# Performance work log

Hardware: AMD Instinct MI355X
Metric: run time of the kernel (lower is better)

Reference implementation:

```python
import jax, jax.numpy as jnp
import numpy as np

L = 262144      # number of points
C = 256         # in_channels
NH = 8          # num_heads
G = 64          # group_size
FF = 2048       # torch TransformerEncoderLayer default dim_feedforward
LPAD = 262144   # padded length, divisible by G; LPAD//G divisible by batch_size
BS = 4


def setup_inputs() -> dict:
    key = jax.random.key(0)
    ks = jax.random.split(key, 12)
    def w(k, shape, scale=0.02):
        return jax.random.normal(k, shape, jnp.float32) * scale
    return {
        "feats_flat": jax.random.normal(ks[0], (L, C), jnp.float32),
        "x_idx": jax.random.randint(ks[1], (L,), 0, L),
        "flat2win": jax.random.randint(ks[2], (LPAD,), 0, L),
        "win2flat": jax.random.randint(ks[3], (L,), 0, LPAD),
        "in_proj_w": w(ks[4], (3 * C, C)),
        "in_proj_b": jnp.zeros((3 * C,), jnp.float32),
        "out_proj_w": w(ks[5], (C, C)),
        "out_proj_b": jnp.zeros((C,), jnp.float32),
        "lin1_w": w(ks[6], (FF, C)),
        "lin1_b": jnp.zeros((FF,), jnp.float32),
        "lin2_w": w(ks[7], (C, FF)),
        "lin2_b": jnp.zeros((C,), jnp.float32),
        "ln1_g": jnp.ones((C,), jnp.float32),
        "ln1_b": jnp.zeros((C,), jnp.float32),
        "ln2_g": jnp.ones((C,), jnp.float32),
        "ln2_b": jnp.zeros((C,), jnp.float32),
        "proj_w": w(ks[8], (C, 2 * C)),
        "proj_b": jnp.zeros((C,), jnp.float32),
        "batch_size": BS,
    }


def _layer_norm(x, g, b, eps=1e-5):
    mu = jnp.mean(x, axis=-1, keepdims=True)
    var = jnp.var(x, axis=-1, keepdims=True)
    return (x - mu) * jax.lax.rsqrt(var + eps) * g + b


def _mha(x, in_proj_w, in_proj_b, out_proj_w, out_proj_b):
    B, S, Cm = x.shape
    hd = Cm // NH
    qkv = x @ in_proj_w.T + in_proj_b                      # [B,S,3C]
    q, k, v = jnp.split(qkv, 3, axis=-1)
    q = q.reshape(B, S, NH, hd)
    k = k.reshape(B, S, NH, hd)
    v = v.reshape(B, S, NH, hd)
    scores = jnp.einsum("bqhd,bkhd->bhqk", q, k) / jnp.sqrt(jnp.float32(hd))
    attn = jax.nn.softmax(scores, axis=-1)
    out = jnp.einsum("bhqk,bkhd->bqhd", attn, v).reshape(B, S, Cm)
    return out @ out_proj_w.T + out_proj_b


def reference(feats_flat, x_idx, flat2win, win2flat,
              in_proj_w, in_proj_b, out_proj_w, out_proj_b,
              lin1_w, lin1_b, lin2_w, lin2_b,
              ln1_g, ln1_b, ln2_g, ln2_b,
              proj_w, proj_b, batch_size):
    Cc = feats_flat.shape[1]
    # gather: feats_flat[indices][flat2win] -> [NW, G, C]
    feats_win = feats_flat[x_idx][flat2win].reshape(-1, G, Cc)
    # adaptive max pool over the group axis -> [NW, C]
    feats_pool = jnp.max(feats_win, axis=1)
    # torch TransformerEncoderLayer (post-norm, relu, eval/no-dropout)
    x = feats_pool.reshape(batch_size, -1, Cc)             # [B, S, C]
    x = _layer_norm(x + _mha(x, in_proj_w, in_proj_b, out_proj_w, out_proj_b), ln1_g, ln1_b)
    ff = jax.nn.relu(x @ lin1_w.T + lin1_b) @ lin2_w.T + lin2_b
    x = _layer_norm(x + ff, ln2_g, ln2_b)
    feats_global = x.reshape(-1, Cc)                       # [NW, C]
    # broadcast global feature to every group element, concat (global first)
    fuse_in = jnp.concatenate(
        [jnp.broadcast_to(feats_global[:, None, :], feats_win.shape), feats_win],
        axis=-1)                                           # [NW, G, 2C]
    feats_fuse = (fuse_in @ proj_w.T + proj_b).reshape(-1, Cc)  # [LPAD, C]
    # scatter back: feats_flat[indices] = feats_fuse[win2flat]
    return feats_flat.at[x_idx].set(feats_fuse[win2flat])
```

## Files before the change

kernel.cpp:

```cpp
#include <hip/hip_runtime.h>
#include <math.h>

namespace {
constexpr int kL    = 262144;
constexpr int kC    = 256;
constexpr int kNH   = 8;
constexpr int kG    = 64;
constexpr int kFF   = 2048;
constexpr int kLPAD = 262144;
constexpr int kBS   = 4;
constexpr int kNW   = kLPAD / kG;
constexpr int kS    = kNW / kBS;
constexpr int kHD   = kC / kNH;

constexpr size_t MB        = 1024 * 1024;
constexpr size_t OFF_GIDX   = 0;
constexpr size_t OFF_WINNER = 1 * MB;
constexpr size_t OFF_WLIST  = 2 * MB;
constexpr size_t OFF_CNT    = 3 * MB;
constexpr size_t OFF_X0     = 4 * MB;
constexpr size_t OFF_BASE   = 8 * MB;
constexpr size_t OFF_QKV    = 8 * MB;
constexpr size_t OFF_ATTN   = 20 * MB;
constexpr size_t OFF_X2     = 20 * MB;
constexpr size_t OFF_Y      = 24 * MB;
constexpr size_t OFF_X1     = 28 * MB;
constexpr size_t OFF_FF1    = 32 * MB;
constexpr size_t OFF_WINB   = 64 * MB;
constexpr size_t OFF_WOUTB  = OFF_WINB  + 512 * 1024;
constexpr size_t OFF_W1B    = OFF_WOUTB + 256 * 1024;
constexpr size_t OFF_W2B    = OFF_W1B   + 1536 * 1024;
constexpr size_t OFF_WP1B   = OFF_W2B   + 1536 * 1024;
constexpr size_t OFF_WP2B   = OFF_WP1B  + 256 * 1024;

typedef __attribute__((ext_vector_type(8))) short bf16x8;
typedef __attribute__((ext_vector_type(4))) float f32x4;

__device__ inline unsigned short f2bf(float f) {
  union { float f; unsigned int u; } x; x.f = f;
  unsigned int r = x.u + 0x7fff + ((x.u >> 16) & 1);
  return (unsigned short)(r >> 16);
}
}

__global__ __launch_bounds__(256) void k_winner(const int* __restrict__ x_idx,
                                                int* __restrict__ winner) {
  int i = blockIdx.x * 256 + threadIdx.x;
  atomicMax(&winner[x_idx[i]], i);
}

__global__ __launch_bounds__(256) void k_compact(const int* __restrict__ x_idx,
                                                 const int* __restrict__ winner,
                                                 int* __restrict__ wlist,
                                                 int* __restrict__ cnt) {
  int i = blockIdx.x * 256 + threadIdx.x;
  if (winner[x_idx[i]] == i) {
    int p = atomicAdd(cnt, 1);
    wlist[p] = i;
  }
}

__global__ __launch_bounds__(256) void k_copy(const float* __restrict__ feats,
                                              const int* __restrict__ winner,
                                              float* __restrict__ out) {
  size_t idx = (size_t)blockIdx.x * 256 + threadIdx.x;
  int row = (int)(idx >> 6);
  int c4 = (int)(idx & 63);
  if (winner[row] < 0) {
    *(float4*)&out[(size_t)row * kC + c4 * 4] =
        *(const float4*)&feats[(size_t)row * kC + c4 * 4];
  }
}

__global__ __launch_bounds__(256) void k_pool(const float* __restrict__ feats,
                                              const int* __restrict__ x_idx,
                                              const int* __restrict__ flat2win,
                                              int* __restrict__ gidx,
                                              float* __restrict__ x0) {
  int w = blockIdx.x, t = threadIdx.x;
  __shared__ int rows[kG];
  if (t < kG) {
    int g = x_idx[flat2win[w * kG + t]];
    rows[t] = g;
    gidx[w * kG + t] = g;
  }
  __syncthreads();
  float m = -INFINITY;
  #pragma unroll 4
  for (int g = 0; g < kG; ++g)
    m = fmaxf(m, feats[(size_t)rows[g] * kC + t]);
  x0[w * kC + t] = m;
}

__global__ __launch_bounds__(256) void k_wcast(const float* __restrict__ in_proj_w,
                                               const float* __restrict__ out_proj_w,
                                               const float* __restrict__ lin1_w,
                                               const float* __restrict__ lin2_w,
                                               const float* __restrict__ proj_w,
                                               unsigned short* __restrict__ WINB,
                                               unsigned short* __restrict__ WOUTB,
                                               unsigned short* __restrict__ W1B,
                                               unsigned short* __restrict__ W2B,
                                               unsigned short* __restrict__ WP1,
                                               unsigned short* __restrict__ WP2) {
  int blk = blockIdx.x, t = threadIdx.x;
  const float* src = nullptr; unsigned short* dst = nullptr; int i = 0;
  if (blk < 192)       { src = in_proj_w;  dst = WINB;  i = blk * 256 + t; }
  else if (blk < 256)  { src = out_proj_w; dst = WOUTB; i = (blk - 192) * 256 + t; }
  else if (blk < 768)  { src = lin1_w;     dst = W1B;   i = (blk - 256) * 256 + t; }
  else if (blk < 1280) { src = lin2_w;     dst = W2B;   i = (blk - 768) * 256 + t; }
  else {
    int c = blk - 1280;
    WP1[c * kC + t] = f2bf(proj_w[(size_t)c * (2 * kC) + t]);
    WP2[c * kC + t] = f2bf(proj_w[(size_t)c * (2 * kC) + kC + t]);
    return;
  }
  float4 v = ((const float4*)src)[i];
  ushort4 b;
  b.x = f2bf(v.x); b.y = f2bf(v.y); b.z = f2bf(v.z); b.w = f2bf(v.w);
  ((ushort4*)dst)[i] = b;
}

template <bool RELU>
__global__ __launch_bounds__(256) void k_gemm_bf(const float* __restrict__ A, int lda,
                                                 const unsigned short* __restrict__ Wb,
                                                 const float* __restrict__ bias,
                                                 float* __restrict__ Cc, int ldc,
                                                 int K) {
  const int m0 = blockIdx.y * 64;
  const int nb = blockIdx.x * 256;
  const int t = threadIdx.x;
  const int lane = t & 63, w = t >> 6;
  const int c0 = nb + w * 64;
  const int kb = lane >> 4;
  const int lr = lane & 15;

  __shared__ __align__(16) unsigned short As[64 * 256];

  f32x4 acc[4][4] = {};
  for (int kc = 0; kc < K; kc += 256) {
    #pragma unroll
    for (int i = 0; i < 16; ++i) {
      int row = i * 4 + w;
      float4 f4 = *(const float4*)&A[(size_t)(m0 + row) * lda + kc + lane * 4];
      ushort4 b4;
      b4.x = f2bf(f4.x); b4.y = f2bf(f4.y); b4.z = f2bf(f4.z); b4.w = f2bf(f4.w);
      unsigned int off = (((unsigned)row * 512u) + (unsigned)lane * 8u) ^ (((unsigned)row & 7u) << 4);
      *(ushort4*)((char*)As + off) = b4;
    }
    __syncthreads();

    #pragma unroll
    for (int ks = 0; ks < 8; ++ks) {
      const int k0 = ks * 32;
      bf16x8 a[4], b[4];
      #pragma unroll
      for (int rt = 0; rt < 4; ++rt) {
        int row = rt * 16 + lr;
        unsigned int off = (((unsigned)row * 512u) + (unsigned)(k0 + kb * 8) * 2u) ^
                           (((unsigned)row & 7u) << 4);
        a[rt] = *(const bf16x8*)((const char*)As + off);
      }
      #pragma unroll
      for (int ct = 0; ct < 4; ++ct) {
        int c = c0 + ct * 16 + lr;
        b[ct] = *(const bf16x8*)&Wb[(size_t)c * K + kc + k0 + kb * 8];
      }
      #pragma unroll
      for (int rt = 0; rt < 4; ++rt)
        #pragma unroll
        for (int ct = 0; ct < 4; ++ct)
          acc[rt][ct] = __builtin_amdgcn_mfma_f32_16x16x32_bf16(a[rt], b[ct], acc[rt][ct], 0, 0, 0);
    }
    __syncthreads();
  }

  #pragma unroll
  for (int rt = 0; rt < 4; ++rt) {
    #pragma unroll
    for (int r = 0; r < 4; ++r) {
      int row = m0 + rt * 16 + kb * 4 + r;
      #pragma unroll
      for (int ct = 0; ct < 4; ++ct) {
        int c = c0 + ct * 16 + lr;
        float v = acc[rt][ct][r] + bias[c];
        if (RELU) v = fmaxf(v, 0.f);
        Cc[(size_t)row * ldc + c] = v;
      }
    }
  }
}

__global__ __launch_bounds__(256) void k_qkvt(const float* __restrict__ qkv,
                                              unsigned short* __restrict__ Qh,
                                              unsigned short* __restrict__ Kh,
                                              unsigned short* __restrict__ Vh) {
  const float scale = 0.17677669529663687f;
  int r = blockIdx.x;
  int b = r >> 10, s = r & 1023;
  int t = threadIdx.x;
  int h = t >> 5, d = t & 31;
  size_t src = (size_t)r * (3 * kC);
  size_t dst = (((size_t)(b * kNH + h) * kS) + s) * kHD + d;
  Qh[dst] = f2bf(qkv[src + t] * scale);
  Kh[dst] = f2bf(qkv[src + kC + t]);
  Vh[dst] = f2bf(qkv[src + 2 * kC + t]);
}

__global__ __launch_bounds__(256) void k_attn(const unsigned short* __restrict__ Qh,
                                              const unsigned short* __restrict__ Kh,
                                              const unsigned short* __restrict__ Vh,
                                              float* __restrict__ attn_out) {
  const int q0 = blockIdx.x * 64;
  const int bh = blockIdx.y;
  const int b = bh >> 3, h = bh & 7;
  const int t = threadIdx.x;
  const int lane = t & 63, w = t >> 6;
  const int kb = lane >> 4, lr = lane & 15;

  __shared__ __align__(16) unsigned short Ks[64][40];
  __shared__ __align__(16) unsigned short VTs[32][72];
  __shared__ __align__(16) unsigned short Ps[4][16][72];

  bf16x8 aq = *(const bf16x8*)(Qh + (((size_t)bh * kS) + q0 + w * 16 + lr) * kHD + kb * 8);

  const unsigned short* kbase = Kh + (size_t)bh * kS * kHD;
  const unsigned short* vbase = Vh + (size_t)bh * kS * kHD;

  float m[4], l[4];
  f32x4 O[2] = {};
  #pragma unroll
  for (int r = 0; r < 4; ++r) { m[r] = -INFINITY; l[r] = 0.f; }

  for (int kt = 0; kt < kS / 64; ++kt) {
    {
      int key = t >> 2, d0 = (t & 3) * 8;
      size_t srow = ((size_t)(kt * 64 + key)) * kHD + d0;
      bf16x8 kv = *(const bf16x8*)(kbase + srow);
      *(bf16x8*)&Ks[key][d0] = kv;
      bf16x8 vv = *(const bf16x8*)(vbase + srow);
      #pragma unroll
      for (int i = 0; i < 8; ++i) VTs[d0 + i][key] = (unsigned short)vv[i];
    }
    __syncthreads();

    f32x4 S[4] = {};
    #pragma unroll
    for (int ct = 0; ct < 4; ++ct) {
      bf16x8 bk = *(const bf16x8*)&Ks[ct * 16 + lr][kb * 8];
      S[ct] = __builtin_amdgcn_mfma_f32_16x16x32_bf16(aq, bk, S[ct], 0, 0, 0);
    }

    float alpha[4];
    #pragma unroll
    for (int r = 0; r < 4; ++r) {
      float tmax = fmaxf(fmaxf(S[0][r], S[1][r]), fmaxf(S[2][r], S[3][r]));
      #pragma unroll
      for (int off = 8; off; off >>= 1) tmax = fmaxf(tmax, __shfl_xor(tmax, off, 16));
      float newm = fmaxf(m[r], tmax);
      alpha[r] = __expf(m[r] - newm);
      float p[4], ps = 0.f;
      #pragma unroll
      for (int ct = 0; ct < 4; ++ct) { p[ct] = __expf(S[ct][r] - newm); ps += p[ct]; }
      #pragma unroll
      for (int off = 8; off; off >>= 1) ps += __shfl_xor(ps, off, 16);
      l[r] = l[r] * alpha[r] + ps;
      m[r] = newm;
      #pragma unroll
      for (int ct = 0; ct < 4; ++ct) Ps[w][kb * 4 + r][ct * 16 + lr] = f2bf(p[ct]);
    }
    #pragma unroll
    for (int r = 0; r < 4; ++r) { O[0][r] *= alpha[r]; O[1][r] *= alpha[r]; }

    #pragma unroll
    for (int ks = 0; ks < 2; ++ks) {
      bf16x8 ap = *(const bf16x8*)&Ps[w][lr][ks * 32 + kb * 8];
      #pragma unroll
      for (int ct = 0; ct < 2; ++ct) {
        bf16x8 bv = *(const bf16x8*)&VTs[ct * 16 + lr][ks * 32 + kb * 8];
        O[ct] = __builtin_amdgcn_mfma_f32_16x16x32_bf16(ap, bv, O[ct], 0, 0, 0);
      }
    }
    __syncthreads();
  }

  #pragma unroll
  for (int ct = 0; ct < 2; ++ct) {
    #pragma unroll
    for (int r = 0; r < 4; ++r) {
      size_t row = (size_t)b * kS + q0 + w * 16 + kb * 4 + r;
      attn_out[row * kC + h * kHD + ct * 16 + lr] = O[ct][r] / l[r];
    }
  }
}

__global__ __launch_bounds__(256) void k_ln(const float* __restrict__ Y,
                                            const float* __restrict__ R,
                                            const float* __restrict__ g,
                                            const float* __restrict__ bb,
                                            float* __restrict__ Out) {
  int row = blockIdx.x, t = threadIdx.x;
  int wv = t >> 6, lane = t & 63;
  float v = Y[(size_t)row * kC + t] + R[(size_t)row * kC + t];
  __shared__ float red1[4], red2[4];
  float s = v;
  #pragma unroll
  for (int off = 32; off; off >>= 1) s += __shfl_xor(s, off);
  if (lane == 0) red1[wv] = s;
  __syncthreads();
  float mu = (red1[0] + red1[1] + red1[2] + red1[3]) * (1.0f / kC);
  float d = v - mu;
  float sq = d * d;
  #pragma unroll
  for (int off = 32; off; off >>= 1) sq += __shfl_xor(sq, off);
  if (lane == 0) red2[wv] = sq;
  __syncthreads();
  float var = (red2[0] + red2[1] + red2[2] + red2[3]) * (1.0f / kC);
  Out[(size_t)row * kC + t] = d * rsqrtf(var + 1e-5f) * g[t] + bb[t];
}

__global__ __launch_bounds__(256) void k_fuse(const float* __restrict__ feats,
                                              const int* __restrict__ gidx,
                                              const int* __restrict__ wlist,
                                              const int* __restrict__ cnt,
                                              const int* __restrict__ win2flat,
                                              const int* __restrict__ x_idx,
                                              const float* __restrict__ base,
                                              const unsigned short* __restrict__ W2B,
                                              float* __restrict__ out) {
  const int count = cnt[0];
  const int r0 = blockIdx.x * 64;
  if (r0 >= count) return;
  const int nr = min(64, count - r0);
  const int t = threadIdx.x;
  const int lane = t & 63, w = t >> 6;

  __shared__ __align__(16) unsigned short As[64 * 256];
  __shared__ int dstrow[64], wwin[64], srcrow[64];

  if (t < 64) {
    int rr = min(r0 + t, count - 1);
    int i = wlist[rr];
    int j = win2flat[i];
    srcrow[t] = gidx[j];
    wwin[t] = j >> 6;
    dstrow[t] = x_idx[i];
  }
  __syncthreads();

  for (int i = 0; i < 16; ++i) {
    int row = i * 4 + w;
    float4 f4 = *(const float4*)&feats[(size_t)srcrow[row] * kC + lane * 4];
    ushort4 b4;
    b4.x = f2bf(f4.x); b4.y = f2bf(f4.y); b4.z = f2bf(f4.z); b4.w = f2bf(f4.w);
    unsigned int off = (((unsigned)row * 512u) + (unsigned)lane * 8u) ^ (((unsigned)row & 7u) << 4);
    *(ushort4*)((char*)As + off) = b4;
  }
  __syncthreads();

  const int c0 = w * 64;
  const int kb = lane >> 4;
  const int lr = lane & 15;
  f32x4 acc[4][4] = {};
  for (int ks = 0; ks < 8; ++ks) {
    const int k0 = ks * 32;
    bf16x8 a[4], b[4];
    #pragma unroll
    for (int rt = 0; rt < 4; ++rt) {
      int row = rt * 16 + lr;
      unsigned int off = (((unsigned)row * 512u) + (unsigned)(k0 + kb * 8) * 2u) ^
                         (((unsigned)row & 7u) << 4);
      a[rt] = *(const bf16x8*)((const char*)As + off);
    }
    #pragma unroll
    for (int ct = 0; ct < 4; ++ct) {
      int c = c0 + ct * 16 + lr;
      b[ct] = *(const bf16x8*)&W2B[(size_t)c * kC + k0 + kb * 8];
    }
    #pragma unroll
    for (int rt = 0; rt < 4; ++rt)
      #pragma unroll
      for (int ct = 0; ct < 4; ++ct)
        acc[rt][ct] = __builtin_amdgcn_mfma_f32_16x16x32_bf16(a[rt], b[ct], acc[rt][ct], 0, 0, 0);
  }

  #pragma unroll
  for (int rt = 0; rt < 4; ++rt) {
    #pragma unroll
    for (int r = 0; r < 4; ++r) {
      int row = rt * 16 + kb * 4 + r;
      if (row < nr) {
        size_t orow = (size_t)dstrow[row] * kC;
        size_t brow = (size_t)wwin[row] * kC;
        #pragma unroll
        for (int ct = 0; ct < 4; ++ct) {
          int c = c0 + ct * 16 + lr;
          out[orow + c] = acc[rt][ct][r] + base[brow + c];
        }
      }
    }
  }
}

extern "C" void kernel_launch(void* const* d_in, const int* in_sizes, int n_in,
                              void* d_out, int out_size, void* d_ws, size_t ws_size,
                              hipStream_t stream) {
  const float* feats      = (const float*)d_in[0];
  const int*   x_idx      = (const int*)d_in[1];
  const int*   flat2win   = (const int*)d_in[2];
  const int*   win2flat   = (const int*)d_in[3];
  const float* in_proj_w  = (const float*)d_in[4];
  const float* in_proj_b  = (const float*)d_in[5];
  const float* out_proj_w = (const float*)d_in[6];
  const float* out_proj_b = (const float*)d_in[7];
  const float* lin1_w     = (const float*)d_in[8];
  const float* lin1_b     = (const float*)d_in[9];
  const float* lin2_w     = (const float*)d_in[10];
  const float* lin2_b     = (const float*)d_in[11];
  const float* ln1_g      = (const float*)d_in[12];
  const float* ln1_b      = (const float*)d_in[13];
  const float* ln2_g      = (const float*)d_in[14];
  const float* ln2_b      = (const float*)d_in[15];
  const float* proj_w     = (const float*)d_in[16];
  const float* proj_b     = (const float*)d_in[17];

  char* ws = (char*)d_ws;
  int*   gidx   = (int*)(ws + OFF_GIDX);
  int*   winner = (int*)(ws + OFF_WINNER);
  int*   wlist  = (int*)(ws + OFF_WLIST);
  int*   cnt    = (int*)(ws + OFF_CNT);
  float* x0     = (float*)(ws + OFF_X0);
  float* qkv    = (float*)(ws + OFF_QKV);
  float* attn   = (float*)(ws + OFF_ATTN);
  float* y      = (float*)(ws + OFF_Y);
  float* x1     = (float*)(ws + OFF_X1);
  float* ff1    = (float*)(ws + OFF_FF1);
  float* x2     = (float*)(ws + OFF_X2);
  float* basep  = (float*)(ws + OFF_BASE);
  unsigned short* WINB  = (unsigned short*)(ws + OFF_WINB);
  unsigned short* WOUTB = (unsigned short*)(ws + OFF_WOUTB);
  unsigned short* W1B   = (unsigned short*)(ws + OFF_W1B);
  unsigned short* W2B   = (unsigned short*)(ws + OFF_W2B);
  unsigned short* WP1B  = (unsigned short*)(ws + OFF_WP1B);
  unsigned short* WP2B  = (unsigned short*)(ws + OFF_WP2B);
  float* out    = (float*)d_out;

  unsigned short* Qh = (unsigned short*)(ws + OFF_Y);
  unsigned short* Kh = (unsigned short*)(ws + OFF_Y + 2 * MB);
  unsigned short* Vh = (unsigned short*)(ws + OFF_X1);

  hipMemsetAsync(winner, 0xFF, (size_t)kL * sizeof(int), stream);
  hipMemsetAsync(cnt, 0, sizeof(int), stream);

  k_winner<<<kL / 256, 256, 0, stream>>>(x_idx, winner);
  k_compact<<<kL / 256, 256, 0, stream>>>(x_idx, winner, wlist, cnt);
  k_copy<<<kL / 4, 256, 0, stream>>>(feats, winner, out);
  k_pool<<<kNW, 256, 0, stream>>>(feats, x_idx, flat2win, gidx, x0);
  k_wcast<<<1536, 256, 0, stream>>>(in_proj_w, out_proj_w, lin1_w, lin2_w, proj_w,
                                    WINB, WOUTB, W1B, W2B, WP1B, WP2B);

  k_gemm_bf<false><<<dim3(3, kNW / 64), 256, 0, stream>>>(
      x0, kC, WINB, in_proj_b, qkv, 3 * kC, kC);
  k_qkvt<<<kNW, 256, 0, stream>>>(qkv, Qh, Kh, Vh);
  k_attn<<<dim3(kS / 64, kBS * kNH), 256, 0, stream>>>(Qh, Kh, Vh, attn);
  k_gemm_bf<false><<<dim3(1, kNW / 64), 256, 0, stream>>>(
      attn, kC, WOUTB, out_proj_b, y, kC, kC);
  k_ln<<<kNW, 256, 0, stream>>>(y, x0, ln1_g, ln1_b, x1);
  k_gemm_bf<true><<<dim3(kFF / 256, kNW / 64), 256, 0, stream>>>(
      x1, kC, W1B, lin1_b, ff1, kFF, kC);
  k_gemm_bf<false><<<dim3(1, kNW / 64), 256, 0, stream>>>(
      ff1, kFF, W2B, lin2_b, y, kC, kFF);
  k_ln<<<kNW, 256, 0, stream>>>(y, x1, ln2_g, ln2_b, x2);
  k_gemm_bf<false><<<dim3(1, kNW / 64), 256, 0, stream>>>(
      x2, kC, WP1B, proj_b, basep, kC, kC);
  k_fuse<<<kL / 64, 256, 0, stream>>>(feats, gidx, wlist, cnt, win2flat, x_idx,
                                      basep, WP2B, out);
}
```

Before: 442.5 us.

## Fuse QKV transpose, LayerNorm and final projection into GEMM epilogues; store bf16 intermediates

Folds the QKV head-split transpose and Q scaling into the QKV GEMM epilogue. Fuses the out-proj and FF2 GEMMs with residual-add LayerNorm in 16-row tiles, and chains the proj_w first-half GEMM after LN2 inside the same kernel. The attention output and FF1 activations are stored as bf16 instead of fp32. This removes several kernel launches and fp32 round-trips through global memory. In exchange it uses smaller 16-row GEMM tiles with less weight reuse, and the single-pass variance formula can lose some precision.

```diff
diff --git a/kernel.cpp b/kernel.cpp
--- a/kernel.cpp
+++ b/kernel.cpp
@@ -20,11 +20,11 @@
 constexpr size_t OFF_CNT    = 3 * MB;
 constexpr size_t OFF_X0     = 4 * MB;
 constexpr size_t OFF_BASE   = 8 * MB;
-constexpr size_t OFF_QKV    = 8 * MB;
-constexpr size_t OFF_ATTN   = 20 * MB;
-constexpr size_t OFF_X2     = 20 * MB;
-constexpr size_t OFF_Y      = 24 * MB;
-constexpr size_t OFF_X1     = 28 * MB;
+constexpr size_t OFF_ATTN   = 12 * MB;
+constexpr size_t OFF_QH     = 16 * MB;
+constexpr size_t OFF_KH     = 18 * MB;
+constexpr size_t OFF_VH     = 20 * MB;
+constexpr size_t OFF_X1     = 24 * MB;
 constexpr size_t OFF_FF1    = 32 * MB;
 constexpr size_t OFF_WINB   = 64 * MB;
 constexpr size_t OFF_WOUTB  = OFF_WINB  + 512 * 1024;
@@ -121,96 +121,80 @@
   ((ushort4*)dst)[i] = b;
 }
 
-template <bool RELU>
-__global__ __launch_bounds__(256) void k_gemm_bf(const float* __restrict__ A, int lda,
-                                                 const unsigned short* __restrict__ Wb,
-                                                 const float* __restrict__ bias,
-                                                 float* __restrict__ Cc, int ldc,
-                                                 int K) {
+__global__ __launch_bounds__(256) void k_gemm_qkv(const float* __restrict__ A,
+                                                  const unsigned short* __restrict__ Wb,
+                                                  const float* __restrict__ bias,
+                                                  unsigned short* __restrict__ Qh,
+                                                  unsigned short* __restrict__ Kh,
+                                                  unsigned short* __restrict__ Vh) {
+  const float scale = 0.17677669529663687f;
   const int m0 = blockIdx.y * 64;
-  const int nb = blockIdx.x * 256;
+  const int sec = blockIdx.x;
   const int t = threadIdx.x;
   const int lane = t & 63, w = t >> 6;
-  const int c0 = nb + w * 64;
-  const int kb = lane >> 4;
-  const int lr = lane & 15;
+  const int c0 = w * 64;
+  const int kb = lane >> 4, lr = lane & 15;
 
   __shared__ __align__(16) unsigned short As[64 * 256];
 
   f32x4 acc[4][4] = {};
-  for (int kc = 0; kc < K; kc += 256) {
-    #pragma unroll
-    for (int i = 0; i < 16; ++i) {
-      int row = i * 4 + w;
-      float4 f4 = *(const float4*)&A[(size_t)(m0 + row) * lda + kc + lane * 4];
-      ushort4 b4;
-      b4.x = f2bf(f4.x); b4.y = f2bf(f4.y); b4.z = f2bf(f4.z); b4.w = f2bf(f4.w);
-      unsigned int off = (((unsigned)row * 512u) + (unsigned)lane * 8u) ^ (((unsigned)row & 7u) << 4);
-      *(ushort4*)((char*)As + off) = b4;
-    }
-    __syncthreads();
-
-    #pragma unroll
-    for (int ks = 0; ks < 8; ++ks) {
-      const int k0 = ks * 32;
-      bf16x8 a[4], b[4];
-      #pragma unroll
-      for (int rt = 0; rt < 4; ++rt) {
-        int row = rt * 16 + lr;
-        unsigned int off = (((unsigned)row * 512u) + (unsigned)(k0 + kb * 8) * 2u) ^
-                           (((unsigned)row & 7u) << 4);
-        a[rt] = *(const bf16x8*)((const char*)As + off);
-      }
+  #pragma unroll
+  for (int i = 0; i < 16; ++i) {
+    int row = i * 4 + w;
+    float4 f4 = *(const float4*)&A[(size_t)(m0 + row) * kC + lane * 4];
+    ushort4 b4;
+    b4.x = f2bf(f4.x); b4.y = f2bf(f4.y); b4.z = f2bf(f4.z); b4.w = f2bf(f4.w);
+    unsigned int off = (((unsigned)row * 512u) + (unsigned)lane * 8u) ^ (((unsigned)row & 7u) << 4);
+    *(ushort4*)((char*)As + off) = b4;
+  }
+  __syncthreads();
+
+  #pragma unroll
+  for (int ks = 0; ks < 8; ++ks) {
+    const int k0 = ks * 32;
+    bf16x8 a[4], b[4];
+    #pragma unroll
+    for (int rt = 0; rt < 4; ++rt) {
+      int row = rt * 16 + lr;
+      unsigned int off = (((unsigned)row * 512u) + (unsigned)(k0 + kb * 8) * 2u) ^
+                         (((unsigned)row & 7u) << 4);
+      a[rt] = *(const bf16x8*)((const char*)As + off);
+    }
+    #pragma unroll
+    for (int ct = 0; ct < 4; ++ct) {
+      int c = sec * kC + c0 + ct * 16 + lr;
+      b[ct] = *(const bf16x8*)&Wb[(size_t)c * kC + k0 + kb * 8];
+    }
+    #pragma unroll
+    for (int rt = 0; rt < 4; ++rt)
+      #pragma unroll
+      for (int ct = 0; ct < 4; ++ct)
+        acc[rt][ct] = __builtin_amdgcn_mfma_f32_16x16x32_bf16(a[rt], b[ct], acc[rt][ct], 0, 0, 0);
+  }
+
+  unsigned short* dstbuf = (sec == 0) ? Qh : (sec == 1) ? Kh : Vh;
+  #pragma unroll
+  for (int rt = 0; rt < 4; ++rt) {
+    #pragma unroll
+    for (int r = 0; r < 4; ++r) {
+      int row = m0 + rt * 16 + kb * 4 + r;
+      int bb = row >> 10, s = row & 1023;
       #pragma unroll
       for (int ct = 0; ct < 4; ++ct) {
         int c = c0 + ct * 16 + lr;
-        b[ct] = *(const bf16x8*)&Wb[(size_t)c * K + kc + k0 + kb * 8];
-      }
-      #pragma unroll
-      for (int rt = 0; rt < 4; ++rt)
-        #pragma unroll
-        for (int ct = 0; ct < 4; ++ct)
-          acc[rt][ct] = __builtin_amdgcn_mfma_f32_16x16x32_bf16(a[rt], b[ct], acc[rt][ct], 0, 0, 0);
-    }
-    __syncthreads();
-  }
-
-  #pragma unroll
-  for (int rt = 0; rt < 4; ++rt) {
-    #pragma unroll
-    for (int r = 0; r < 4; ++r) {
-      int row = m0 + rt * 16 + kb * 4 + r;
-      #pragma unroll
-      for (int ct = 0; ct < 4; ++ct) {
-        int c = c0 + ct * 16 + lr;
-        float v = acc[rt][ct][r] + bias[c];
-        if (RELU) v = fmaxf(v, 0.f);
-        Cc[(size_t)row * ldc + c] = v;
-      }
-    }
-  }
-}
-
-__global__ __launch_bounds__(256) void k_qkvt(const float* __restrict__ qkv,
-                                              unsigned short* __restrict__ Qh,
-                                              unsigned short* __restrict__ Kh,
-                                              unsigned short* __restrict__ Vh) {
-  const float scale = 0.17677669529663687f;
-  int r = blockIdx.x;
-  int b = r >> 10, s = r & 1023;
-  int t = threadIdx.x;
-  int h = t >> 5, d = t & 31;
-  size_t src = (size_t)r * (3 * kC);
-  size_t dst = (((size_t)(b * kNH + h) * kS) + s) * kHD + d;
-  Qh[dst] = f2bf(qkv[src + t] * scale);
-  Kh[dst] = f2bf(qkv[src + kC + t]);
-  Vh[dst] = f2bf(qkv[src + 2 * kC + t]);
+        float v = acc[rt][ct][r] + bias[sec * kC + c];
+        if (sec == 0) v *= scale;
+        int h = c >> 5, d = c & 31;
+        dstbuf[(((size_t)(bb * kNH + h) * kS) + s) * kHD + d] = f2bf(v);
+      }
+    }
+  }
 }
 
 __global__ __launch_bounds__(256) void k_attn(const unsigned short* __restrict__ Qh,
                                               const unsigned short* __restrict__ Kh,
                                               const unsigned short* __restrict__ Vh,
-                                              float* __restrict__ attn_out) {
+                                              unsigned short* __restrict__ attn_out) {
   const int q0 = blockIdx.x * 64;
   const int bh = blockIdx.y;
   const int b = bh >> 3, h = bh & 7;
@@ -289,34 +273,195 @@
     #pragma unroll
     for (int r = 0; r < 4; ++r) {
       size_t row = (size_t)b * kS + q0 + w * 16 + kb * 4 + r;
-      attn_out[row * kC + h * kHD + ct * 16 + lr] = O[ct][r] / l[r];
-    }
-  }
-}
-
-__global__ __launch_bounds__(256) void k_ln(const float* __restrict__ Y,
-                                            const float* __restrict__ R,
-                                            const float* __restrict__ g,
-                                            const float* __restrict__ bb,
-                                            float* __restrict__ Out) {
-  int row = blockIdx.x, t = threadIdx.x;
-  int wv = t >> 6, lane = t & 63;
-  float v = Y[(size_t)row * kC + t] + R[(size_t)row * kC + t];
-  __shared__ float red1[4], red2[4];
-  float s = v;
-  #pragma unroll
-  for (int off = 32; off; off >>= 1) s += __shfl_xor(s, off);
-  if (lane == 0) red1[wv] = s;
+      attn_out[row * kC + h * kHD + ct * 16 + lr] = f2bf(O[ct][r] / l[r]);
+    }
+  }
+}
+
+template <bool DO_BASE>
+__global__ __launch_bounds__(256) void k_gemm_ln(const unsigned short* __restrict__ A,
+                                                 int K,
+                                                 const unsigned short* __restrict__ Wb,
+                                                 const float* __restrict__ bias,
+                                                 const float* __restrict__ R,
+                                                 const float* __restrict__ g,
+                                                 const float* __restrict__ bb,
+                                                 float* __restrict__ Out,
+                                                 const unsigned short* __restrict__ WbB,
+                                                 const float* __restrict__ biasB) {
+  const int m0 = blockIdx.x * 16;
+  const int t = threadIdx.x;
+  const int lane = t & 63, w = t >> 6;
+  const int c0 = w * 64;
+  const int kb = lane >> 4, lr = lane & 15;
+
+  __shared__ __align__(16) unsigned short As[16 * 256];
+  __shared__ __align__(16) unsigned short Xs[16 * 256];
+  __shared__ float red[2][16][4];
+
+  f32x4 acc[4] = {};
+  for (int kc = 0; kc < K; kc += 256) {
+    #pragma unroll
+    for (int i = 0; i < 2; ++i) {
+      int idx = i * 256 + t;
+      int row = idx >> 5, seg = idx & 31;
+      bf16x8 v = *(const bf16x8*)&A[(size_t)(m0 + row) * K + kc + seg * 8];
+      unsigned int off = (((unsigned)row * 512u) + (unsigned)seg * 16u) ^ (((unsigned)row & 7u) << 4);
+      *(bf16x8*)((char*)As + off) = v;
+    }
+    __syncthreads();
+
+    #pragma unroll
+    for (int ks = 0; ks < 8; ++ks) {
+      const int k0 = ks * 32;
+      unsigned int aoff = (((unsigned)lr * 512u) + (unsigned)(k0 + kb * 8) * 2u) ^
+                          (((unsigned)lr & 7u) << 4);
+      bf16x8 a = *(const bf16x8*)((const char*)As + aoff);
+      #pragma unroll
+      for (int ct = 0; ct < 4; ++ct) {
+        bf16x8 b = *(const bf16x8*)&Wb[(size_t)(c0 + ct * 16 + lr) * K + kc + k0 + kb * 8];
+        acc[ct] = __builtin_amdgcn_mfma_f32_16x16x32_bf16(a, b, acc[ct], 0, 0, 0);
+      }
+    }
+    __syncthreads();
+  }
+
+  float v[4][4];
+  float s[4], sq[4];
+  #pragma unroll
+  for (int r = 0; r < 4; ++r) { s[r] = 0.f; sq[r] = 0.f; }
+  #pragma unroll
+  for (int r = 0; r < 4; ++r) {
+    int row = m0 + kb * 4 + r;
+    #pragma unroll
+    for (int ct = 0; ct < 4; ++ct) {
+      int c = c0 + ct * 16 + lr;
+      float x = acc[ct][r] + bias[c] + R[(size_t)row * kC + c];
+      v[r][ct] = x;
+      s[r] += x;
+      sq[r] += x * x;
+    }
+  }
+  #pragma unroll
+  for (int r = 0; r < 4; ++r) {
+    #pragma unroll
+    for (int off = 8; off; off >>= 1) {
+      s[r]  += __shfl_xor(s[r], off, 16);
+      sq[r] += __shfl_xor(sq[r], off, 16);
+    }
+    if (lr == 0) { red[0][kb * 4 + r][w] = s[r]; red[1][kb * 4 + r][w] = sq[r]; }
+  }
   __syncthreads();
-  float mu = (red1[0] + red1[1] + red1[2] + red1[3]) * (1.0f / kC);
-  float d = v - mu;
-  float sq = d * d;
-  #pragma unroll
-  for (int off = 32; off; off >>= 1) sq += __shfl_xor(sq, off);
-  if (lane == 0) red2[wv] = sq;
+
+  #pragma unroll
+  for (int r = 0; r < 4; ++r) {
+    int lrow = kb * 4 + r;
+    float su = red[0][lrow][0] + red[0][lrow][1] + red[0][lrow][2] + red[0][lrow][3];
+    float sg = red[1][lrow][0] + red[1][lrow][1] + red[1][lrow][2] + red[1][lrow][3];
+    float mu = su * (1.0f / kC);
+    float var = sg * (1.0f / kC) - mu * mu;
+    float rs = rsqrtf(var + 1e-5f);
+    #pragma unroll
+    for (int ct = 0; ct < 4; ++ct) {
+      int c = c0 + ct * 16 + lr;
+      float yv = (v[r][ct] - mu) * rs * g[c] + bb[c];
+      if (!DO_BASE) {
+        Out[(size_t)(m0 + lrow) * kC + c] = yv;
+      } else {
+        unsigned int off = (((unsigned)lrow * 512u) + (unsigned)c * 2u) ^ (((unsigned)lrow & 7u) << 4);
+        *(unsigned short*)((char*)Xs + off) = f2bf(yv);
+      }
+    }
+  }
+
+  if (DO_BASE) {
+    __syncthreads();
+    f32x4 acc2[4] = {};
+    #pragma unroll
+    for (int ks = 0; ks < 8; ++ks) {
+      const int k0 = ks * 32;
+      unsigned int aoff = (((unsigned)lr * 512u) + (unsigned)(k0 + kb * 8) * 2u) ^
+                          (((unsigned)lr & 7u) << 4);
+      bf16x8 a = *(const bf16x8*)((const char*)Xs + aoff);
+      #pragma unroll
+      for (int ct = 0; ct < 4; ++ct) {
+        bf16x8 b = *(const bf16x8*)&WbB[(size_t)(c0 + ct * 16 + lr) * kC + k0 + kb * 8];
+        acc2[ct] = __builtin_amdgcn_mfma_f32_16x16x32_bf16(a, b, acc2[ct], 0, 0, 0);
+      }
+    }
+    #pragma unroll
+    for (int r = 0; r < 4; ++r) {
+      int row = m0 + kb * 4 + r;
+      #pragma unroll
+      for (int ct = 0; ct < 4; ++ct) {
+        int c = c0 + ct * 16 + lr;
+        Out[(size_t)row * kC + c] = acc2[ct][r] + biasB[c];
+      }
+    }
+  }
+}
+
+__global__ __launch_bounds__(256) void k_gemm_ff1(const float* __restrict__ A,
+                                                  const unsigned short* __restrict__ Wb,
+                                                  const float* __restrict__ bias,
+                                                  unsigned short* __restrict__ Cc) {
+  const int m0 = blockIdx.y * 64;
+  const int nb = blockIdx.x * 256;
+  const int t = threadIdx.x;
+  const int lane = t & 63, w = t >> 6;
+  const int c0 = nb + w * 64;
+  const int kb = lane >> 4, lr = lane & 15;
+
+  __shared__ __align__(16) unsigned short As[64 * 256];
+
+  f32x4 acc[4][4] = {};
+  #pragma unroll
+  for (int i = 0; i < 16; ++i) {
+    int row = i * 4 + w;
+    float4 f4 = *(const float4*)&A[(size_t)(m0 + row) * kC + lane * 4];
+    ushort4 b4;
+    b4.x = f2bf(f4.x); b4.y = f2bf(f4.y); b4.z = f2bf(f4.z); b4.w = f2bf(f4.w);
+    unsigned int off = (((unsigned)row * 512u) + (unsigned)lane * 8u) ^ (((unsigned)row & 7u) << 4);
+    *(ushort4*)((char*)As + off) = b4;
+  }
   __syncthreads();
-  float var = (red2[0] + red2[1] + red2[2] + red2[3]) * (1.0f / kC);
-  Out[(size_t)row * kC + t] = d * rsqrtf(var + 1e-5f) * g[t] + bb[t];
+
+  #pragma unroll
+  for (int ks = 0; ks < 8; ++ks) {
+    const int k0 = ks * 32;
+    bf16x8 a[4], b[4];
+    #pragma unroll
+    for (int rt = 0; rt < 4; ++rt) {
+      int row = rt * 16 + lr;
+      unsigned int off = (((unsigned)row * 512u) + (unsigned)(k0 + kb * 8) * 2u) ^
+                         (((unsigned)row & 7u) << 4);
+      a[rt] = *(const bf16x8*)((const char*)As + off);
+    }
+    #pragma unroll
+    for (int ct = 0; ct < 4; ++ct) {
+      int c = c0 + ct * 16 + lr;
+      b[ct] = *(const bf16x8*)&Wb[(size_t)c * kC + k0 + kb * 8];
+    }
+    #pragma unroll
+    for (int rt = 0; rt < 4; ++rt)
+      #pragma unroll
+      for (int ct = 0; ct < 4; ++ct)
+        acc[rt][ct] = __builtin_amdgcn_mfma_f32_16x16x32_bf16(a[rt], b[ct], acc[rt][ct], 0, 0, 0);
+  }
+
+  #pragma unroll
+  for (int rt = 0; rt < 4; ++rt) {
+    #pragma unroll
+    for (int r = 0; r < 4; ++r) {
+      int row = m0 + rt * 16 + kb * 4 + r;
+      #pragma unroll
+      for (int ct = 0; ct < 4; ++ct) {
+        int c = c0 + ct * 16 + lr;
+        float vv = fmaxf(acc[rt][ct][r] + bias[c], 0.f);
+        Cc[(size_t)row * kFF + c] = f2bf(vv);
+      }
+    }
+  }
 }
 
 __global__ __launch_bounds__(256) void k_fuse(const float* __restrict__ feats,
@@ -430,13 +575,13 @@
   int*   wlist  = (int*)(ws + OFF_WLIST);
   int*   cnt    = (int*)(ws + OFF_CNT);
   float* x0     = (float*)(ws + OFF_X0);
-  float* qkv    = (float*)(ws + OFF_QKV);
-  float* attn   = (float*)(ws + OFF_ATTN);
-  float* y      = (float*)(ws + OFF_Y);
+  float* basep  = (float*)(ws + OFF_BASE);
   float* x1     = (float*)(ws + OFF_X1);
-  float* ff1    = (float*)(ws + OFF_FF1);
-  float* x2     = (float*)(ws + OFF_X2);
-  float* basep  = (float*)(ws + OFF_BASE);
+  unsigned short* attnb = (unsigned short*)(ws + OFF_ATTN);
+  unsigned short* Qh    = (unsigned short*)(ws + OFF_QH);
+  unsigned short* Kh    = (unsigned short*)(ws + OFF_KH);
+  unsigned short* Vh    = (unsigned short*)(ws + OFF_VH);
+  unsigned short* ff1b  = (unsigned short*)(ws + OFF_FF1);
   unsigned short* WINB  = (unsigned short*)(ws + OFF_WINB);
   unsigned short* WOUTB = (unsigned short*)(ws + OFF_WOUTB);
   unsigned short* W1B   = (unsigned short*)(ws + OFF_W1B);
@@ -445,10 +590,6 @@
   unsigned short* WP2B  = (unsigned short*)(ws + OFF_WP2B);
   float* out    = (float*)d_out;
 
-  unsigned short* Qh = (unsigned short*)(ws + OFF_Y);
-  unsigned short* Kh = (unsigned short*)(ws + OFF_Y + 2 * MB);
-  unsigned short* Vh = (unsigned short*)(ws + OFF_X1);
-
   hipMemsetAsync(winner, 0xFF, (size_t)kL * sizeof(int), stream);
   hipMemsetAsync(cnt, 0, sizeof(int), stream);
 
@@ -459,20 +600,13 @@
   k_wcast<<<1536, 256, 0, stream>>>(in_proj_w, out_proj_w, lin1_w, lin2_w, proj_w,
                                     WINB, WOUTB, W1B, W2B, WP1B, WP2B);
 
-  k_gemm_bf<false><<<dim3(3, kNW / 64), 256, 0, stream>>>(
-      x0, kC, WINB, in_proj_b, qkv, 3 * kC, kC);
-  k_qkvt<<<kNW, 256, 0, stream>>>(qkv, Qh, Kh, Vh);
-  k_attn<<<dim3(kS / 64, kBS * kNH), 256, 0, stream>>>(Qh, Kh, Vh, attn);
-  k_gemm_bf<false><<<dim3(1, kNW / 64), 256, 0, stream>>>(
-      attn, kC, WOUTB, out_proj_b, y, kC, kC);
-  k_ln<<<kNW, 256, 0, stream>>>(y, x0, ln1_g, ln1_b, x1);
-  k_gemm_bf<true><<<dim3(kFF / 256, kNW / 64), 256, 0, stream>>>(
-      x1, kC, W1B, lin1_b, ff1, kFF, kC);
-  k_gemm_bf<false><<<dim3(1, kNW / 64), 256, 0, stream>>>(
-      ff1, kFF, W2B, lin2_b, y, kC, kFF);
-  k_ln<<<kNW, 256, 0, stream>>>(y, x1, ln2_g, ln2_b, x2);
-  k_gemm_bf<false><<<dim3(1, kNW / 64), 256, 0, stream>>>(
-      x2, kC, WP1B, proj_b, basep, kC, kC);
+  k_gemm_qkv<<<dim3(3, kNW / 64), 256, 0, stream>>>(x0, WINB, in_proj_b, Qh, Kh, Vh);
+  k_attn<<<dim3(kS / 64, kBS * kNH), 256, 0, stream>>>(Qh, Kh, Vh, attnb);
+  k_gemm_ln<false><<<kNW / 16, 256, 0, stream>>>(
+      attnb, kC, WOUTB, out_proj_b, x0, ln1_g, ln1_b, x1, nullptr, nullptr);
+  k_gemm_ff1<<<dim3(kFF / 256, kNW / 64), 256, 0, stream>>>(x1, W1B, lin1_b, ff1b);
+  k_gemm_ln<true><<<kNW / 16, 256, 0, stream>>>(
+      ff1b, kFF, W2B, lin2_b, x1, ln2_g, ln2_b, basep, WP1B, proj_b);
   k_fuse<<<kL / 64, 256, 0, stream>>>(feats, gidx, wlist, cnt, win2flat, x_idx,
                                       basep, WP2B, out);
 }
```

Measured after the change: 404.1 us. 1.09x faster.
